# Performance work log

Hardware: AMD Instinct MI355X
Metric: run time of the kernel (lower is better)

The kernel has to match this reference:

```python
import jax, jax.numpy as jnp
import numpy as np

EPS = 1e-8  # torch.nn.CosineSimilarity default eps


def setup_inputs() -> dict:
    key = jax.random.key(0)
    N, D = 8192, 256
    x = jax.random.normal(key, (N, D), dtype=jnp.float32)
    return {"input": x}


def reference(input) -> jnp.ndarray:
    # Cosine similarity between all pairs of rows. Equivalent to the
    # repeat_interleave/repeat construction, but computed as a normalized
    # Gram matrix (same math: cos(x_i, x_j) with norm clamped at eps).
    n = input.shape[0]
    norms = jnp.maximum(jnp.linalg.norm(input, axis=1, keepdims=True), EPS)
    xn = input / norms                                   # [N, D]
    cos_mat = jnp.einsum('id,jd->ij', xn, xn)            # [N, N]
    n_f = jnp.float32(n)
    simloss = (jnp.sum(jnp.square(cos_mat)) - n_f) / (n_f * n_f - n_f)
    return simloss
```

## Files before the change

kernel.cpp:

```cpp
#include <hip/hip_runtime.h>

#define D 256
#define TILE 64
#define NPAIRS 10
#define CHUNK 512
#define EPS 1e-8f

typedef __attribute__((ext_vector_type(8))) short bf16x8;
typedef __attribute__((ext_vector_type(4))) float f32x4;

__device__ __forceinline__ void pair_decode(int p, int& ta, int& tb) {
  if (p < 4)      { ta = 0; tb = p; }
  else if (p < 7) { ta = 1; tb = p - 3; }
  else if (p < 9) { ta = 2; tb = p - 5; }
  else            { ta = 3; tb = 3; }
}

__device__ __forceinline__ int swz(int col, int r) {
  int g = ((col >> 2) & 7) ^ ((col & 3) << 1);
  return col * 64 + (r ^ (g << 3));
}

__device__ __forceinline__ unsigned short rne_bf16(float f) {
  unsigned u = __float_as_uint(f);
  return (unsigned short)((u + 0x7fffu + ((u >> 16) & 1u)) >> 16);
}

__global__ __launch_bounds__(256) void k_prep(
    const float* __restrict__ x, float* __restrict__ inv,
    float* __restrict__ S, unsigned int* __restrict__ cnt, int N) {
  if (blockIdx.x == 0 && threadIdx.x == 0) { *S = 0.0f; *cnt = 0u; }
  int wave = (blockIdx.x * blockDim.x + threadIdx.x) >> 6;
  int lane = threadIdx.x & 63;
  if (wave >= N) return;
  const float4 v = reinterpret_cast<const float4*>(x + (size_t)wave * D)[lane];
  float s = v.x * v.x + v.y * v.y + v.z * v.z + v.w * v.w;
  #pragma unroll
  for (int o = 32; o > 0; o >>= 1) s += __shfl_xor(s, o);
  if (lane == 0) inv[wave] = 1.0f / fmaxf(sqrtf(s), EPS);
}

__global__ __launch_bounds__(512) void k_gram(
    const float* __restrict__ x, const float* __restrict__ inv,
    float* __restrict__ slabs, int nchunk) {
  int ta, tb; pair_decode(blockIdx.x, ta, tb);
  const bool same = (ta == tb);
  const int row0 = blockIdx.y * CHUNK;

  __shared__ short X[128 * 64];
  const int tid = threadIdx.x;

  const int lcb = same ? 4 : 5;
  const int ntask = 16 << lcb;
  const bool active = tid < ntask;
  const int c0 = (tid & ((1 << lcb) - 1)) << 2;
  const int r0 = (active ? (tid >> lcb) : 0) << 2;
  const int gc0 = (c0 < TILE) ? ta * TILE + c0 : tb * TILE + (c0 - TILE);

  const int w = tid >> 6, lane = tid & 63;
  const int i0 = (w >> 1) << 4;
  const int j0 = (w & 1) << 5;
  const int lm = lane & 15, lk = lane >> 4;
  const int bbase = same ? 0 : 64;

  f32x4 zero = {0.f, 0.f, 0.f, 0.f};
  f32x4 acc[2] = {zero, zero};

  float4 pv[4]; float4 piv;
  if (active) {
    piv = *reinterpret_cast<const float4*>(&inv[row0 + r0]);
    const float* xb = x + (size_t)(row0 + r0) * D + gc0;
    #pragma unroll
    for (int jj = 0; jj < 4; ++jj)
      pv[jj] = *reinterpret_cast<const float4*>(xb + (size_t)jj * D);
  }

  const int NSUB = CHUNK / 64;
  for (int s = 0; s < NSUB; ++s) {
    if (active) {
      const float ivv[4] = {piv.x, piv.y, piv.z, piv.w};
      unsigned short hh[4][4];
      #pragma unroll
      for (int jj = 0; jj < 4; ++jj) {
        const float vv[4] = {pv[jj].x, pv[jj].y, pv[jj].z, pv[jj].w};
        #pragma unroll
        for (int cc = 0; cc < 4; ++cc)
          hh[jj][cc] = rne_bf16(vv[cc] * ivv[jj]);
      }
      #pragma unroll
      for (int cc = 0; cc < 4; ++cc)
        *reinterpret_cast<ushort4*>(&X[swz(c0 + cc, r0)]) =
            make_ushort4(hh[0][cc], hh[1][cc], hh[2][cc], hh[3][cc]);
      if (s + 1 < NSUB) {
        const int nr0 = row0 + (s + 1) * 64 + r0;
        piv = *reinterpret_cast<const float4*>(&inv[nr0]);
        const float* xb = x + (size_t)nr0 * D + gc0;
        #pragma unroll
        for (int jj = 0; jj < 4; ++jj)
          pv[jj] = *reinterpret_cast<const float4*>(xb + (size_t)jj * D);
      }
    }
    __syncthreads();
    #pragma unroll
    for (int rr = 0; rr < 64; rr += 32) {
      const int rbase = rr + lk * 8;
      bf16x8 A  = *reinterpret_cast<const bf16x8*>(&X[swz(i0 + lm, rbase)]);
      bf16x8 B0 = *reinterpret_cast<const bf16x8*>(&X[swz(bbase + j0 + lm, rbase)]);
      bf16x8 B1 = *reinterpret_cast<const bf16x8*>(&X[swz(bbase + j0 + 16 + lm, rbase)]);
      acc[0] = __builtin_amdgcn_mfma_f32_16x16x32_bf16(A, B0, acc[0], 0, 0, 0);
      acc[1] = __builtin_amdgcn_mfma_f32_16x16x32_bf16(A, B1, acc[1], 0, 0, 0);
    }
    __syncthreads();
  }

  float* slab = slabs +
      ((size_t)blockIdx.x * nchunk + blockIdx.y) * (TILE * TILE);
  #pragma unroll
  for (int jt = 0; jt < 2; ++jt)
    #pragma unroll
    for (int rg = 0; rg < 4; ++rg)
      slab[(i0 + lk * 4 + rg) * TILE + (j0 + jt * 16 + lm)] = acc[jt][rg];
}

__global__ __launch_bounds__(256) void k_reduce(
    const float* __restrict__ slabs, float* __restrict__ S,
    unsigned int* __restrict__ cnt, float* __restrict__ out,
    int nchunk, int N, int nblocks) {
  const int g = blockIdx.x * 256 + threadIdx.x;
  const int p = g >> 12;
  const int e = g & 4095;
  const float* base = slabs + (size_t)p * nchunk * (TILE * TILE) + e;
  float tot = 0.f;
  #pragma unroll 4
  for (int c = 0; c < nchunk; ++c) tot += base[(size_t)c * (TILE * TILE)];
  const bool diag = (p == 0) | (p == 4) | (p == 7) | (p == 9);
  float part = (diag ? 1.f : 2.f) * tot * tot;
  #pragma unroll
  for (int o = 32; o > 0; o >>= 1) part += __shfl_xor(part, o);
  __shared__ float red[4];
  int lane = threadIdx.x & 63, w = threadIdx.x >> 6;
  if (lane == 0) red[w] = part;
  __syncthreads();
  if (threadIdx.x == 0) {
    float blk = red[0] + red[1] + red[2] + red[3];
    atomicAdd(S, blk);
    __threadfence();
    unsigned int old = atomicAdd(cnt, 1u);
    if (old == (unsigned int)(nblocks - 1)) {
      float Sv = __hip_atomic_load(S, __ATOMIC_RELAXED,
                                   __HIP_MEMORY_SCOPE_AGENT);
      float nf = (float)N;
      out[0] = (Sv - nf) / (nf * nf - nf);
    }
  }
}

extern "C" void kernel_launch(void* const* d_in, const int* in_sizes, int n_in,
                              void* d_out, int out_size, void* d_ws, size_t ws_size,
                              hipStream_t stream) {
  const float* x = (const float*)d_in[0];
  float* out = (float*)d_out;
  const int N = in_sizes[0] / D;
  const int nchunk = N / CHUNK;

  float* inv = (float*)d_ws;
  float* Sp = inv + N;
  unsigned int* cnt = (unsigned int*)(Sp + 1);
  float* slabs = inv + N + 64;

  k_prep<<<dim3(N / 4), dim3(256), 0, stream>>>(x, inv, Sp, cnt, N);
  k_gram<<<dim3(NPAIRS, nchunk), dim3(512), 0, stream>>>(x, inv, slabs, nchunk);
  const int nb = NPAIRS * (TILE * TILE / 256);
  k_reduce<<<dim3(nb), dim3(256), 0, stream>>>(slabs, Sp, cnt, out,
                                               nchunk, N, nb);
}
```

Measured before the change: 25.81 us.

## Fuse norm, Gram, and reduce kernels into one persistent kernel with grid barriers

Merges the three launches (row-norm prep, tiled Gram MFMA, slab reduction) into one kernel of 160 blocks that synchronise through two atomic grid barriers. Inverse norms are staged in shared memory per chunk, and control words are zeroed with a memset. This removes two kernel launch gaps and their inter-kernel idle time. In exchange it adds barrier spin latency and relies on all 160 blocks being co-resident, and the memset is an extra stream operation.

```diff
diff --git a/kernel.cpp b/kernel.cpp
--- a/kernel.cpp
+++ b/kernel.cpp
@@ -4,6 +4,8 @@
 #define TILE 64
 #define NPAIRS 10
 #define CHUNK 512
+#define NCHUNK 16
+#define NBLK 160
 #define EPS 1e-8f
 
 typedef __attribute__((ext_vector_type(8))) short bf16x8;
@@ -26,29 +28,49 @@
   return (unsigned short)((u + 0x7fffu + ((u >> 16) & 1u)) >> 16);
 }
 
-__global__ __launch_bounds__(256) void k_prep(
-    const float* __restrict__ x, float* __restrict__ inv,
-    float* __restrict__ S, unsigned int* __restrict__ cnt, int N) {
-  if (blockIdx.x == 0 && threadIdx.x == 0) { *S = 0.0f; *cnt = 0u; }
-  int wave = (blockIdx.x * blockDim.x + threadIdx.x) >> 6;
-  int lane = threadIdx.x & 63;
-  if (wave >= N) return;
-  const float4 v = reinterpret_cast<const float4*>(x + (size_t)wave * D)[lane];
-  float s = v.x * v.x + v.y * v.y + v.z * v.z + v.w * v.w;
-  #pragma unroll
-  for (int o = 32; o > 0; o >>= 1) s += __shfl_xor(s, o);
-  if (lane == 0) inv[wave] = 1.0f / fmaxf(sqrtf(s), EPS);
+__device__ __forceinline__ void gridbar(unsigned int* bar) {
+  __syncthreads();
+  if (threadIdx.x == 0) {
+    __hip_atomic_fetch_add(bar, 1u, __ATOMIC_RELEASE,
+                           __HIP_MEMORY_SCOPE_AGENT);
+    while (__hip_atomic_load(bar, __ATOMIC_ACQUIRE,
+                             __HIP_MEMORY_SCOPE_AGENT) < (unsigned)NBLK)
+      __builtin_amdgcn_s_sleep(2);
+  }
+  __syncthreads();
 }
 
-__global__ __launch_bounds__(512) void k_gram(
-    const float* __restrict__ x, const float* __restrict__ inv,
-    float* __restrict__ slabs, int nchunk) {
-  int ta, tb; pair_decode(blockIdx.x, ta, tb);
+__global__ __launch_bounds__(512) void k_main(
+    const float* __restrict__ x, float* __restrict__ ws_inv,
+    float* __restrict__ slabs, float* __restrict__ S,
+    unsigned int* __restrict__ cnt, unsigned int* __restrict__ bar1,
+    unsigned int* __restrict__ bar2, float* __restrict__ out, int N) {
+  const int bx = blockIdx.x;
+  const int pair = bx >> 4, chunk = bx & 15;
+  int ta, tb; pair_decode(pair, ta, tb);
   const bool same = (ta == tb);
-  const int row0 = blockIdx.y * CHUNK;
+  const int row0 = chunk * CHUNK;
+  const int tid = threadIdx.x;
+  const int w = tid >> 6, lane = tid & 63;
 
   __shared__ short X[128 * 64];
-  const int tid = threadIdx.x;
+  __shared__ float inv_s[CHUNK];
+  __shared__ float red[4];
+
+  for (int r = bx * 8 + w; r < N; r += NBLK * 8) {
+    const float4 v = reinterpret_cast<const float4*>(x + (size_t)r * D)[lane];
+    float s = v.x * v.x + v.y * v.y + v.z * v.z + v.w * v.w;
+    #pragma unroll
+    for (int o = 32; o > 0; o >>= 1) s += __shfl_xor(s, o);
+    if (lane == 0)
+      __hip_atomic_store(&ws_inv[r], 1.0f / fmaxf(sqrtf(s), EPS),
+                         __ATOMIC_RELAXED, __HIP_MEMORY_SCOPE_AGENT);
+  }
+  gridbar(bar1);
+
+  inv_s[tid] = __hip_atomic_load(&ws_inv[row0 + tid], __ATOMIC_RELAXED,
+                                 __HIP_MEMORY_SCOPE_AGENT);
+  __syncthreads();
 
   const int lcb = same ? 4 : 5;
   const int ntask = 16 << lcb;
@@ -57,7 +79,6 @@
   const int r0 = (active ? (tid >> lcb) : 0) << 2;
   const int gc0 = (c0 < TILE) ? ta * TILE + c0 : tb * TILE + (c0 - TILE);
 
-  const int w = tid >> 6, lane = tid & 63;
   const int i0 = (w >> 1) << 4;
   const int j0 = (w & 1) << 5;
   const int lm = lane & 15, lk = lane >> 4;
@@ -66,9 +87,8 @@
   f32x4 zero = {0.f, 0.f, 0.f, 0.f};
   f32x4 acc[2] = {zero, zero};
 
-  float4 pv[4]; float4 piv;
+  float4 pv[4];
   if (active) {
-    piv = *reinterpret_cast<const float4*>(&inv[row0 + r0]);
     const float* xb = x + (size_t)(row0 + r0) * D + gc0;
     #pragma unroll
     for (int jj = 0; jj < 4; ++jj)
@@ -78,23 +98,21 @@
   const int NSUB = CHUNK / 64;
   for (int s = 0; s < NSUB; ++s) {
     if (active) {
-      const float ivv[4] = {piv.x, piv.y, piv.z, piv.w};
       unsigned short hh[4][4];
       #pragma unroll
       for (int jj = 0; jj < 4; ++jj) {
+        const float iv = inv_s[s * 64 + r0 + jj];
         const float vv[4] = {pv[jj].x, pv[jj].y, pv[jj].z, pv[jj].w};
         #pragma unroll
         for (int cc = 0; cc < 4; ++cc)
-          hh[jj][cc] = rne_bf16(vv[cc] * ivv[jj]);
+          hh[jj][cc] = rne_bf16(vv[cc] * iv);
       }
       #pragma unroll
       for (int cc = 0; cc < 4; ++cc)
         *reinterpret_cast<ushort4*>(&X[swz(c0 + cc, r0)]) =
             make_ushort4(hh[0][cc], hh[1][cc], hh[2][cc], hh[3][cc]);
       if (s + 1 < NSUB) {
-        const int nr0 = row0 + (s + 1) * 64 + r0;
-        piv = *reinterpret_cast<const float4*>(&inv[nr0]);
-        const float* xb = x + (size_t)nr0 * D + gc0;
+        const float* xb = x + (size_t)(row0 + (s + 1) * 64 + r0) * D + gc0;
         #pragma unroll
         for (int jj = 0; jj < 4; ++jj)
           pv[jj] = *reinterpret_cast<const float4*>(xb + (size_t)jj * D);
@@ -113,40 +131,38 @@
     __syncthreads();
   }
 
-  float* slab = slabs +
-      ((size_t)blockIdx.x * nchunk + blockIdx.y) * (TILE * TILE);
+  float* slab = slabs + (size_t)bx * (TILE * TILE);
   #pragma unroll
   for (int jt = 0; jt < 2; ++jt)
     #pragma unroll
     for (int rg = 0; rg < 4; ++rg)
-      slab[(i0 + lk * 4 + rg) * TILE + (j0 + jt * 16 + lm)] = acc[jt][rg];
-}
+      __hip_atomic_store(&slab[(i0 + lk * 4 + rg) * TILE + (j0 + jt * 16 + lm)],
+                         acc[jt][rg], __ATOMIC_RELAXED,
+                         __HIP_MEMORY_SCOPE_AGENT);
+  gridbar(bar2);
 
-__global__ __launch_bounds__(256) void k_reduce(
-    const float* __restrict__ slabs, float* __restrict__ S,
-    unsigned int* __restrict__ cnt, float* __restrict__ out,
-    int nchunk, int N, int nblocks) {
-  const int g = blockIdx.x * 256 + threadIdx.x;
-  const int p = g >> 12;
-  const int e = g & 4095;
-  const float* base = slabs + (size_t)p * nchunk * (TILE * TILE) + e;
-  float tot = 0.f;
-  #pragma unroll 4
-  for (int c = 0; c < nchunk; ++c) tot += base[(size_t)c * (TILE * TILE)];
-  const bool diag = (p == 0) | (p == 4) | (p == 7) | (p == 9);
-  float part = (diag ? 1.f : 2.f) * tot * tot;
-  #pragma unroll
-  for (int o = 32; o > 0; o >>= 1) part += __shfl_xor(part, o);
-  __shared__ float red[4];
-  int lane = threadIdx.x & 63, w = threadIdx.x >> 6;
-  if (lane == 0) red[w] = part;
+  float part = 0.f;
+  if (tid < 256) {
+    const int e = ((bx * 256 + tid) & 4095);
+    const float* base = slabs + (size_t)(pair * NCHUNK) * (TILE * TILE) + e;
+    float tot = 0.f;
+    #pragma unroll
+    for (int c = 0; c < NCHUNK; ++c)
+      tot += __hip_atomic_load(&base[(size_t)c * (TILE * TILE)],
+                               __ATOMIC_RELAXED, __HIP_MEMORY_SCOPE_AGENT);
+    const bool diag = (pair == 0) | (pair == 4) | (pair == 7) | (pair == 9);
+    part = (diag ? 1.f : 2.f) * tot * tot;
+    #pragma unroll
+    for (int o = 32; o > 0; o >>= 1) part += __shfl_xor(part, o);
+    if (lane == 0) red[w] = part;
+  }
   __syncthreads();
-  if (threadIdx.x == 0) {
+  if (tid == 0) {
     float blk = red[0] + red[1] + red[2] + red[3];
     atomicAdd(S, blk);
     __threadfence();
     unsigned int old = atomicAdd(cnt, 1u);
-    if (old == (unsigned int)(nblocks - 1)) {
+    if (old == (unsigned int)(NBLK - 1)) {
       float Sv = __hip_atomic_load(S, __ATOMIC_RELAXED,
                                    __HIP_MEMORY_SCOPE_AGENT);
       float nf = (float)N;
@@ -161,16 +177,16 @@
   const float* x = (const float*)d_in[0];
   float* out = (float*)d_out;
   const int N = in_sizes[0] / D;
-  const int nchunk = N / CHUNK;
 
   float* inv = (float*)d_ws;
-  float* Sp = inv + N;
-  unsigned int* cnt = (unsigned int*)(Sp + 1);
-  float* slabs = inv + N + 64;
+  float* ctrl = inv + N;
+  float* S = ctrl;
+  unsigned int* cnt = (unsigned int*)(ctrl + 1);
+  unsigned int* bar1 = (unsigned int*)(ctrl + 2);
+  unsigned int* bar2 = (unsigned int*)(ctrl + 3);
+  float* slabs = ctrl + 64;
 
-  k_prep<<<dim3(N / 4), dim3(256), 0, stream>>>(x, inv, Sp, cnt, N);
-  k_gram<<<dim3(NPAIRS, nchunk), dim3(512), 0, stream>>>(x, inv, slabs, nchunk);
-  const int nb = NPAIRS * (TILE * TILE / 256);
-  k_reduce<<<dim3(nb), dim3(256), 0, stream>>>(slabs, Sp, cnt, out,
-                                               nchunk, N, nb);
+  hipMemsetAsync(ctrl, 0, 16, stream);
+  k_main<<<dim3(NBLK), dim3(512), 0, stream>>>(
+      x, inv, slabs, S, cnt, bar1, bar2, out, N);
 }
```

New measurement: 44.43 us. +72.1%, slower.

## Fuse row-norm computation into gram kernel and double-buffer LDS tile

Applied to the files above, without the earlier changes.

Removes the separate norm kernel: each gram block recomputes inverse norms for its 512-row chunk into shared memory before the main loop. The LDS tile is double-buffered so one barrier per sub-iteration can be dropped, and the chunk count becomes a compile-time constant. This saves a kernel launch and a global round-trip for the norms. In exchange every pair block (10x redundantly) rereads the full chunk rows to compute norms, and the grid is hardwired to N=8192.

```diff
diff --git a/kernel.cpp b/kernel.cpp
--- a/kernel.cpp
+++ b/kernel.cpp
@@ -4,6 +4,7 @@
 #define TILE 64
 #define NPAIRS 10
 #define CHUNK 512
+#define NCHUNK 16
 #define EPS 1e-8f
 
 typedef __attribute__((ext_vector_type(8))) short bf16x8;
@@ -26,29 +27,38 @@
   return (unsigned short)((u + 0x7fffu + ((u >> 16) & 1u)) >> 16);
 }
 
-__global__ __launch_bounds__(256) void k_prep(
-    const float* __restrict__ x, float* __restrict__ inv,
-    float* __restrict__ S, unsigned int* __restrict__ cnt, int N) {
-  if (blockIdx.x == 0 && threadIdx.x == 0) { *S = 0.0f; *cnt = 0u; }
-  int wave = (blockIdx.x * blockDim.x + threadIdx.x) >> 6;
-  int lane = threadIdx.x & 63;
-  if (wave >= N) return;
-  const float4 v = reinterpret_cast<const float4*>(x + (size_t)wave * D)[lane];
-  float s = v.x * v.x + v.y * v.y + v.z * v.z + v.w * v.w;
-  #pragma unroll
-  for (int o = 32; o > 0; o >>= 1) s += __shfl_xor(s, o);
-  if (lane == 0) inv[wave] = 1.0f / fmaxf(sqrtf(s), EPS);
-}
-
 __global__ __launch_bounds__(512) void k_gram(
-    const float* __restrict__ x, const float* __restrict__ inv,
-    float* __restrict__ slabs, int nchunk) {
+    const float* __restrict__ x, float* __restrict__ slabs,
+    float* __restrict__ S, unsigned int* __restrict__ cnt) {
   int ta, tb; pair_decode(blockIdx.x, ta, tb);
   const bool same = (ta == tb);
   const int row0 = blockIdx.y * CHUNK;
+  const int tid = threadIdx.x;
+  const int w = tid >> 6, lane = tid & 63;
 
-  __shared__ short X[128 * 64];
-  const int tid = threadIdx.x;
+  if (blockIdx.x == 0 && blockIdx.y == 0 && tid == 0) { *S = 0.f; *cnt = 0u; }
+
+  __shared__ short X[2][128 * 64];
+  __shared__ float inv_s[CHUNK];
+
+  #pragma unroll
+  for (int g = 0; g < 8; ++g) {
+    float4 v[8];
+    #pragma unroll
+    for (int j = 0; j < 8; ++j)
+      v[j] = reinterpret_cast<const float4*>(
+          x + (size_t)(row0 + w * 64 + g * 8 + j) * D)[lane];
+    #pragma unroll
+    for (int j = 0; j < 8; ++j) {
+      float s = v[j].x * v[j].x + v[j].y * v[j].y +
+                v[j].z * v[j].z + v[j].w * v[j].w;
+      #pragma unroll
+      for (int o = 32; o > 0; o >>= 1) s += __shfl_xor(s, o);
+      if (lane == 0)
+        inv_s[w * 64 + g * 8 + j] = 1.0f / fmaxf(sqrtf(s), EPS);
+    }
+  }
+  __syncthreads();
 
   const int lcb = same ? 4 : 5;
   const int ntask = 16 << lcb;
@@ -57,7 +67,6 @@
   const int r0 = (active ? (tid >> lcb) : 0) << 2;
   const int gc0 = (c0 < TILE) ? ta * TILE + c0 : tb * TILE + (c0 - TILE);
 
-  const int w = tid >> 6, lane = tid & 63;
   const int i0 = (w >> 1) << 4;
   const int j0 = (w & 1) << 5;
   const int lm = lane & 15, lk = lane >> 4;
@@ -66,9 +75,8 @@
   f32x4 zero = {0.f, 0.f, 0.f, 0.f};
   f32x4 acc[2] = {zero, zero};
 
-  float4 pv[4]; float4 piv;
+  float4 pv[4];
   if (active) {
-    piv = *reinterpret_cast<const float4*>(&inv[row0 + r0]);
     const float* xb = x + (size_t)(row0 + r0) * D + gc0;
     #pragma unroll
     for (int jj = 0; jj < 4; ++jj)
@@ -77,24 +85,23 @@
 
   const int NSUB = CHUNK / 64;
   for (int s = 0; s < NSUB; ++s) {
+    short* Xb = X[s & 1];
     if (active) {
-      const float ivv[4] = {piv.x, piv.y, piv.z, piv.w};
       unsigned short hh[4][4];
       #pragma unroll
       for (int jj = 0; jj < 4; ++jj) {
+        const float iv = inv_s[s * 64 + r0 + jj];
         const float vv[4] = {pv[jj].x, pv[jj].y, pv[jj].z, pv[jj].w};
         #pragma unroll
         for (int cc = 0; cc < 4; ++cc)
-          hh[jj][cc] = rne_bf16(vv[cc] * ivv[jj]);
+          hh[jj][cc] = rne_bf16(vv[cc] * iv);
       }
       #pragma unroll
       for (int cc = 0; cc < 4; ++cc)
-        *reinterpret_cast<ushort4*>(&X[swz(c0 + cc, r0)]) =
+        *reinterpret_cast<ushort4*>(&Xb[swz(c0 + cc, r0)]) =
             make_ushort4(hh[0][cc], hh[1][cc], hh[2][cc], hh[3][cc]);
       if (s + 1 < NSUB) {
-        const int nr0 = row0 + (s + 1) * 64 + r0;
-        piv = *reinterpret_cast<const float4*>(&inv[nr0]);
-        const float* xb = x + (size_t)nr0 * D + gc0;
+        const float* xb = x + (size_t)(row0 + (s + 1) * 64 + r0) * D + gc0;
         #pragma unroll
         for (int jj = 0; jj < 4; ++jj)
           pv[jj] = *reinterpret_cast<const float4*>(xb + (size_t)jj * D);
@@ -104,17 +111,16 @@
     #pragma unroll
     for (int rr = 0; rr < 64; rr += 32) {
       const int rbase = rr + lk * 8;
-      bf16x8 A  = *reinterpret_cast<const bf16x8*>(&X[swz(i0 + lm, rbase)]);
-      bf16x8 B0 = *reinterpret_cast<const bf16x8*>(&X[swz(bbase + j0 + lm, rbase)]);
-      bf16x8 B1 = *reinterpret_cast<const bf16x8*>(&X[swz(bbase + j0 + 16 + lm, rbase)]);
+      bf16x8 A  = *reinterpret_cast<const bf16x8*>(&Xb[swz(i0 + lm, rbase)]);
+      bf16x8 B0 = *reinterpret_cast<const bf16x8*>(&Xb[swz(bbase + j0 + lm, rbase)]);
+      bf16x8 B1 = *reinterpret_cast<const bf16x8*>(&Xb[swz(bbase + j0 + 16 + lm, rbase)]);
       acc[0] = __builtin_amdgcn_mfma_f32_16x16x32_bf16(A, B0, acc[0], 0, 0, 0);
       acc[1] = __builtin_amdgcn_mfma_f32_16x16x32_bf16(A, B1, acc[1], 0, 0, 0);
     }
-    __syncthreads();
   }
 
   float* slab = slabs +
-      ((size_t)blockIdx.x * nchunk + blockIdx.y) * (TILE * TILE);
+      ((size_t)blockIdx.x * NCHUNK + blockIdx.y) * (TILE * TILE);
   #pragma unroll
   for (int jt = 0; jt < 2; ++jt)
     #pragma unroll
@@ -125,14 +131,14 @@
 __global__ __launch_bounds__(256) void k_reduce(
     const float* __restrict__ slabs, float* __restrict__ S,
     unsigned int* __restrict__ cnt, float* __restrict__ out,
-    int nchunk, int N, int nblocks) {
+    int N, int nblocks) {
   const int g = blockIdx.x * 256 + threadIdx.x;
   const int p = g >> 12;
   const int e = g & 4095;
-  const float* base = slabs + (size_t)p * nchunk * (TILE * TILE) + e;
+  const float* base = slabs + (size_t)p * NCHUNK * (TILE * TILE) + e;
   float tot = 0.f;
-  #pragma unroll 4
-  for (int c = 0; c < nchunk; ++c) tot += base[(size_t)c * (TILE * TILE)];
+  #pragma unroll
+  for (int c = 0; c < NCHUNK; ++c) tot += base[(size_t)c * (TILE * TILE)];
   const bool diag = (p == 0) | (p == 4) | (p == 7) | (p == 9);
   float part = (diag ? 1.f : 2.f) * tot * tot;
   #pragma unroll
@@ -161,16 +167,13 @@
   const float* x = (const float*)d_in[0];
   float* out = (float*)d_out;
   const int N = in_sizes[0] / D;
-  const int nchunk = N / CHUNK;
 
-  float* inv = (float*)d_ws;
-  float* Sp = inv + N;
-  unsigned int* cnt = (unsigned int*)(Sp + 1);
-  float* slabs = inv + N + 64;
+  float* ctrl = (float*)d_ws;
+  float* S = ctrl;
+  unsigned int* cnt = (unsigned int*)(ctrl + 1);
+  float* slabs = ctrl + 64;
 
-  k_prep<<<dim3(N / 4), dim3(256), 0, stream>>>(x, inv, Sp, cnt, N);
-  k_gram<<<dim3(NPAIRS, nchunk), dim3(512), 0, stream>>>(x, inv, slabs, nchunk);
+  k_gram<<<dim3(NPAIRS, NCHUNK), dim3(512), 0, stream>>>(x, slabs, S, cnt);
   const int nb = NPAIRS * (TILE * TILE / 256);
-  k_reduce<<<dim3(nb), dim3(256), 0, stream>>>(slabs, Sp, cnt, out,
-                                               nchunk, N, nb);
+  k_reduce<<<dim3(nb), dim3(256), 0, stream>>>(slabs, S, cnt, out, N, nb);
 }
```

Result: slower. 41.02 us (+58.9%).

## Rebalance Gram blocks with uneven chunking and double-buffer shared tiles

Applied to the files above, without the earlier changes.

Off-diagonal tile pairs now use 256-row chunks (32 blocks each) and diagonal pairs keep 512-row chunks (16 each), so the grid grows from 160 to 256 blocks with more even per-block work. The shared staging buffer is double-buffered, which drops the trailing barrier in each sub-iteration. The reduce kernel uses a per-pair lookup table for slab offsets and chunk counts. The gain is better CU occupancy on a 256-CU part, at the cost of more slab traffic for the reduce and twice the LDS per block. N is now effectively hardcoded to 8192.

```diff
diff --git a/kernel.cpp b/kernel.cpp
--- a/kernel.cpp
+++ b/kernel.cpp
@@ -2,8 +2,6 @@
 
 #define D 256
 #define TILE 64
-#define NPAIRS 10
-#define CHUNK 512
 #define EPS 1e-8f
 
 typedef __attribute__((ext_vector_type(8))) short bf16x8;
@@ -28,8 +26,8 @@
 
 __global__ __launch_bounds__(256) void k_prep(
     const float* __restrict__ x, float* __restrict__ inv,
-    float* __restrict__ S, unsigned int* __restrict__ cnt, int N) {
-  if (blockIdx.x == 0 && threadIdx.x == 0) { *S = 0.0f; *cnt = 0u; }
+    float* __restrict__ ctrl, int N) {
+  if (blockIdx.x == 0 && threadIdx.x < 16) ctrl[threadIdx.x] = 0.0f;
   int wave = (blockIdx.x * blockDim.x + threadIdx.x) >> 6;
   int lane = threadIdx.x & 63;
   if (wave >= N) return;
@@ -42,13 +40,25 @@
 
 __global__ __launch_bounds__(512) void k_gram(
     const float* __restrict__ x, const float* __restrict__ inv,
-    float* __restrict__ slabs, int nchunk) {
-  int ta, tb; pair_decode(blockIdx.x, ta, tb);
-  const bool same = (ta == tb);
-  const int row0 = blockIdx.y * CHUNK;
+    float* __restrict__ slabs) {
+  const int bid = blockIdx.x;
+  int p, row0, nsub;
+  bool same;
+  if (bid < 192) {
+    const int op[6] = {1, 2, 3, 5, 6, 8};
+    p = op[bid >> 5];
+    row0 = (bid & 31) * 256;  nsub = 4;  same = false;
+  } else {
+    const int dp[4] = {0, 4, 7, 9};
+    p = dp[(bid - 192) >> 4];
+    row0 = ((bid - 192) & 15) * 512;  nsub = 8;  same = true;
+  }
+  int ta, tb; pair_decode(p, ta, tb);
 
-  __shared__ short X[128 * 64];
   const int tid = threadIdx.x;
+  const int w = tid >> 6, lane = tid & 63;
+
+  __shared__ short X[2][128 * 64];
 
   const int lcb = same ? 4 : 5;
   const int ntask = 16 << lcb;
@@ -57,7 +67,6 @@
   const int r0 = (active ? (tid >> lcb) : 0) << 2;
   const int gc0 = (c0 < TILE) ? ta * TILE + c0 : tb * TILE + (c0 - TILE);
 
-  const int w = tid >> 6, lane = tid & 63;
   const int i0 = (w >> 1) << 4;
   const int j0 = (w & 1) << 5;
   const int lm = lane & 15, lk = lane >> 4;
@@ -75,8 +84,8 @@
       pv[jj] = *reinterpret_cast<const float4*>(xb + (size_t)jj * D);
   }
 
-  const int NSUB = CHUNK / 64;
-  for (int s = 0; s < NSUB; ++s) {
+  for (int s = 0; s < nsub; ++s) {
+    short* Xb = X[s & 1];
     if (active) {
       const float ivv[4] = {piv.x, piv.y, piv.z, piv.w};
       unsigned short hh[4][4];
@@ -89,9 +98,9 @@
       }
       #pragma unroll
       for (int cc = 0; cc < 4; ++cc)
-        *reinterpret_cast<ushort4*>(&X[swz(c0 + cc, r0)]) =
+        *reinterpret_cast<ushort4*>(&Xb[swz(c0 + cc, r0)]) =
             make_ushort4(hh[0][cc], hh[1][cc], hh[2][cc], hh[3][cc]);
-      if (s + 1 < NSUB) {
+      if (s + 1 < nsub) {
         const int nr0 = row0 + (s + 1) * 64 + r0;
         piv = *reinterpret_cast<const float4*>(&inv[nr0]);
         const float* xb = x + (size_t)nr0 * D + gc0;
@@ -104,17 +113,15 @@
     #pragma unroll
     for (int rr = 0; rr < 64; rr += 32) {
       const int rbase = rr + lk * 8;
-      bf16x8 A  = *reinterpret_cast<const bf16x8*>(&X[swz(i0 + lm, rbase)]);
-      bf16x8 B0 = *reinterpret_cast<const bf16x8*>(&X[swz(bbase + j0 + lm, rbase)]);
-      bf16x8 B1 = *reinterpret_cast<const bf16x8*>(&X[swz(bbase + j0 + 16 + lm, rbase)]);
+      bf16x8 A  = *reinterpret_cast<const bf16x8*>(&Xb[swz(i0 + lm, rbase)]);
+      bf16x8 B0 = *reinterpret_cast<const bf16x8*>(&Xb[swz(bbase + j0 + lm, rbase)]);
+      bf16x8 B1 = *reinterpret_cast<const bf16x8*>(&Xb[swz(bbase + j0 + 16 + lm, rbase)]);
       acc[0] = __builtin_amdgcn_mfma_f32_16x16x32_bf16(A, B0, acc[0], 0, 0, 0);
       acc[1] = __builtin_amdgcn_mfma_f32_16x16x32_bf16(A, B1, acc[1], 0, 0, 0);
     }
-    __syncthreads();
   }
 
-  float* slab = slabs +
-      ((size_t)blockIdx.x * nchunk + blockIdx.y) * (TILE * TILE);
+  float* slab = slabs + (size_t)bid * (TILE * TILE);
   #pragma unroll
   for (int jt = 0; jt < 2; ++jt)
     #pragma unroll
@@ -125,15 +132,17 @@
 __global__ __launch_bounds__(256) void k_reduce(
     const float* __restrict__ slabs, float* __restrict__ S,
     unsigned int* __restrict__ cnt, float* __restrict__ out,
-    int nchunk, int N, int nblocks) {
+    int N, int nblocks) {
   const int g = blockIdx.x * 256 + threadIdx.x;
   const int p = g >> 12;
   const int e = g & 4095;
-  const float* base = slabs + (size_t)p * nchunk * (TILE * TILE) + e;
+  const int base_tbl[10] = {192, 0, 32, 64, 208, 96, 128, 224, 160, 240};
+  const bool diag = (p == 0) | (p == 4) | (p == 7) | (p == 9);
+  const int nc = diag ? 16 : 32;
+  const float* base = slabs + (size_t)base_tbl[p] * (TILE * TILE) + e;
   float tot = 0.f;
-  #pragma unroll 4
-  for (int c = 0; c < nchunk; ++c) tot += base[(size_t)c * (TILE * TILE)];
-  const bool diag = (p == 0) | (p == 4) | (p == 7) | (p == 9);
+  #pragma unroll 8
+  for (int c = 0; c < nc; ++c) tot += base[(size_t)c * (TILE * TILE)];
   float part = (diag ? 1.f : 2.f) * tot * tot;
   #pragma unroll
   for (int o = 32; o > 0; o >>= 1) part += __shfl_xor(part, o);
@@ -161,16 +170,15 @@
   const float* x = (const float*)d_in[0];
   float* out = (float*)d_out;
   const int N = in_sizes[0] / D;
-  const int nchunk = N / CHUNK;
 
   float* inv = (float*)d_ws;
-  float* Sp = inv + N;
-  unsigned int* cnt = (unsigned int*)(Sp + 1);
-  float* slabs = inv + N + 64;
+  float* ctrl = inv + N;
+  float* S = ctrl;
+  unsigned int* cnt = (unsigned int*)(ctrl + 1);
+  float* slabs = ctrl + 64;
 
-  k_prep<<<dim3(N / 4), dim3(256), 0, stream>>>(x, inv, Sp, cnt, N);
-  k_gram<<<dim3(NPAIRS, nchunk), dim3(512), 0, stream>>>(x, inv, slabs, nchunk);
-  const int nb = NPAIRS * (TILE * TILE / 256);
-  k_reduce<<<dim3(nb), dim3(256), 0, stream>>>(slabs, Sp, cnt, out,
-                                               nchunk, N, nb);
+  k_prep<<<dim3(N / 4), dim3(256), 0, stream>>>(x, inv, ctrl, N);
+  k_gram<<<dim3(256), dim3(512), 0, stream>>>(x, inv, slabs);
+  const int nb = 10 * (TILE * TILE / 256);
+  k_reduce<<<dim3(nb), dim3(256), 0, stream>>>(slabs, S, cnt, out, N, nb);
 }
```

Measured after the change: 26.45 us. +2.5%, slower.
